# Kernel optimization log

Hardware: AMD Instinct MI355X
Metric: run time of the kernel (lower is better)

## Reference

```python
import jax, jax.numpy as jnp
from jax import lax
import numpy as np

P = 7            # patch_size
NP = 10          # n_patches
WIN = 20         # window_size
STRIDE = 4       # window loop stride
EMB = 128        # embedding_dimension
L = WIN - P + 1  # valid-conv output side (14)
HALF = WIN // 2 - P // 2  # window start offset before clipping (7)


def _positions(H, W):
    # x outer, y inner, exactly matching the nested python loops in the source
    return np.array([(x, y) for x in range(0, H - WIN + 1, STRIDE)
                     for y in range(0, W - WIN + 1, STRIDE)], dtype=np.int32)


def _forward(images, Wp, bp, pos_emb, Wb, bb):
    B, C, H, W = images.shape
    BC = B * C
    pos = jnp.asarray(_positions(H, W))  # [Ppos, 2]

    def per_pos(p):
        x, y = p[0], p[1]
        xb0 = jnp.maximum(x - HALF, 0)          # clipped window start (x / cols)
        yb0 = jnp.maximum(y - HALF, 0)          # clipped window start (y / rows)
        winW = jnp.minimum(x - HALF + WIN, W) - xb0  # clipped window width
        winH = jnp.minimum(y - HALF + WIN, H) - yb0  # clipped window height
        # reference patch: rows y:y+P, cols x:x+P (from ORIGINAL data, as in source)
        ref = lax.dynamic_slice(images, (0, 0, y, x), (B, C, P, P)).reshape(BC, 1, P, P)
        # fixed-size window slice; upper bound never clips for our dims, lower-clip
        # handled by masking invalid candidate offsets below
        win = lax.dynamic_slice(images, (0, 0, yb0, xb0), (B, C, WIN, WIN)).reshape(BC, WIN, WIN)
        # grouped cross-correlation == torch conv2d(groups=BC) similarity
        sim = lax.conv_general_dilated(win[None], ref, (1, 1), 'VALID',
                                       feature_group_count=BC,
                                       dimension_numbers=('NCHW', 'OIHW', 'NCHW'))[0]  # [BC,L,L]
        valid = (jnp.arange(L)[:, None] <= winH - P) & (jnp.arange(L)[None, :] <= winW - P)
        sim = jnp.where(valid[None], sim, -jnp.inf)
        _, idx = lax.top_k(sim.reshape(BC, L * L), NP)  # [BC, NP]
        oy, ox = idx // L, idx % L  # row / col offsets inside the window

        def extract(w2, a, b):
            # source's meshgrid indexing yields the TRANSPOSED patch, flattened
            return lax.dynamic_slice(w2, (a, b), (P, P)).T.reshape(P * P)
        patches = jax.vmap(jax.vmap(extract, in_axes=(None, 0, 0)))(win, oy, ox)  # [BC,NP,P*P]
        # source bug kept: x_coords = row offset + x window start (and vice versa)
        return patches, oy + xb0, ox + yb0

    patches, xi, yi = jax.vmap(per_pos)(pos)  # [Ppos,BC,NP,49], [Ppos,BC,NP] int32 x2

    # NOTE: the TransformerEncoder output is discarded in the source; the actual
    # math is back_projection(projection(patches) + pos_emb).
    emb = patches.reshape(-1, B, C, NP, P * P) @ Wp + bp + pos_emb  # [Ppos,B,C,NP,EMB]
    den = (emb @ Wb + bb).reshape(-1, BC, NP, P, P)                 # [Ppos,BC,NP,P,P]

    img0 = images.reshape(BC, H, W)
    cnt0 = jnp.ones((BC, H, W), images.dtype)

    def upd(im, cn, x_i, y_i, d):
        reg = lax.dynamic_slice(im, (y_i, x_i), (P, P))
        c = lax.dynamic_slice(cn, (y_i, x_i), (P, P))
        im = lax.dynamic_update_slice(im, (reg * c + d) / (c + 1.0), (y_i, x_i))
        # source bug kept: counter incremented at transposed slice [x, y]
        ct = lax.dynamic_slice(cn, (x_i, y_i), (P, P)) + 1.0
        cn = lax.dynamic_update_slice(cn, ct, (x_i, y_i))
        return im, cn
    vupd = jax.vmap(upd)  # (b,c) planes are independent -> vectorize

    def n_step(carry, t):
        d, x_i, y_i = t
        return vupd(carry[0], carry[1], x_i, y_i, d), None

    def pos_step(carry, t):
        d, x_i, y_i = t  # d:[BC,NP,P,P]
        carry, _ = lax.scan(n_step, carry, (jnp.moveaxis(d, 1, 0), x_i.T, y_i.T))
        return carry, None

    (img, _), _ = lax.scan(pos_step, (img0, cnt0), (den, xi, yi))
    return img.reshape(B, C, H, W)


def setup_inputs() -> dict:
    key = jax.random.key(0)
    k0, k1, k2, k3 = jax.random.split(key, 4)
    B, C, H, W = 4, 8, 160, 160
    return {
        'images': jax.random.normal(k0, (B, C, H, W), jnp.float32),
        'Wp': jax.random.normal(k1, (P * P, EMB), jnp.float32) * 0.05,
        'bp': jnp.zeros((EMB,), jnp.float32),
        'pos_emb': jax.random.normal(k2, (1, NP, EMB), jnp.float32),
        'Wb': jax.random.normal(k3, (EMB, P * P), jnp.float32) * 0.05,
        'bb': jnp.zeros((P * P,), jnp.float32),
    }


def reference(images, Wp, bp, pos_emb, Wb, bb):
    return _forward(images, Wp, bp, pos_emb, Wb, bb)
```

## Files before the change

### kernel.cpp

```cpp
#include <hip/hip_runtime.h>

#define PS 7
#define NP 10
#define WIN 20
#define STR 4
#define LL 14
#define HALF 7
#define HH 160
#define WW 160
#define BCN 32
#define NX 36
#define PPOS 1296
#define EMBD 128
#define NTASK (BCN * PPOS * NP)
#define NEV (PPOS * NP)
#define CAP 512
#define NTILE 400

__global__ __launch_bounds__(256) void k_mk(const float* __restrict__ Wp,
                                            const float* __restrict__ bp,
                                            const float* __restrict__ pe,
                                            const float* __restrict__ Wb,
                                            const float* __restrict__ bb,
                                            float* __restrict__ M,
                                            float* __restrict__ K,
                                            unsigned long long* __restrict__ MT) {
    int t = blockIdx.x * 256 + threadIdx.x;
    if (t < 49 * 49) {
        int k = t / 49, d = t % 49;
        float acc = 0.f;
        for (int e = 0; e < EMBD; ++e) acc += Wp[k * EMBD + e] * Wb[e * 49 + d];
        M[t] = acc;
    } else if (t < 49 * 49 + NP * 49) {
        int u = t - 49 * 49;
        int n = u / 49, d = u % 49;
        float acc = bb[d];
        for (int e = 0; e < EMBD; ++e) acc += (bp[e] + pe[n * EMBD + e]) * Wb[e * 49 + d];
        K[u] = acc;
    } else if (t < 49 * 49 + NP * 49 + 256) {
        int u = t - (49 * 49 + NP * 49);
        int ey = (u >> 4) - 7, ex = (u & 15) - 7;
        int r0 = ey > 0 ? ey : 0, r1 = ey + 6 < 7 ? ey + 6 : 7;
        int c0 = ex > 0 ? ex : 0, c1 = ex + 6 < 7 ? ex + 6 : 7;
        unsigned long long m = 0ull;
        if (r0 <= r1 && c0 <= c1) {
            unsigned colp = ((1u << (c1 - c0 + 1)) - 1u) << c0;
            for (int rr = r0; rr <= r1; ++rr)
                m |= (unsigned long long)colp << (8 * rr);
        }
        MT[u] = m;
    }
}

__device__ __forceinline__ float dpp_wave_max(float x) {
    int xi = __float_as_int(x);
#define DPP_STEP(ctrl)                                                          \
    {                                                                           \
        int t_ = __builtin_amdgcn_update_dpp(xi, xi, ctrl, 0xf, 0xf, false);    \
        xi = __float_as_int(fmaxf(__int_as_float(xi), __int_as_float(t_)));     \
    }
    DPP_STEP(0x111)
    DPP_STEP(0x112)
    DPP_STEP(0x114)
    DPP_STEP(0x118)
    DPP_STEP(0x142)
    DPP_STEP(0x143)
#undef DPP_STEP
    return __int_as_float(xi);
}

__global__ __launch_bounds__(256) void k_sim(const float* __restrict__ img,
                                             const float* __restrict__ Mg,
                                             const float* __restrict__ Kg,
                                             unsigned* __restrict__ xy,
                                             float* __restrict__ pd) {
    int tid  = threadIdx.x;
    int wv   = __builtin_amdgcn_readfirstlane(tid >> 6);
    int lane = tid & 63;
    int gt   = blockIdx.x * 4 + wv;
    int pos  = gt % PPOS;
    int bc   = gt / PPOS;
    int ix = pos / NX, iy = pos % NX;
    int x = ix * STR, y = iy * STR;
    int xb0 = max(x - HALF, 0), yb0 = max(y - HALF, 0);
    int jmax = x + 6 - xb0;
    int imax = y + 6 - yb0;
    const float* plane = img + bc * (HH * WW);

    float rf[49];
#pragma unroll
    for (int a = 0; a < PS; ++a)
#pragma unroll
        for (int b = 0; b < PS; ++b)
            rf[a * 7 + b] = plane[(y + a) * WW + (x + b)];

    int B = lane;
    bool bval = B < 56;
    int gr = B / 14, c = B % 14;
    int r0 = gr * 4;
    float acc[4] = {0.f, 0.f, 0.f, 0.f};
    const float* wb = plane + yb0 * WW + xb0 + c;
#pragma unroll
    for (int a = 0; a < 10; ++a) {
        int ra = min(r0 + a, 19);
        const float* rp = wb + ra * WW;
#pragma unroll
        for (int b = 0; b < 7; ++b) {
            float tap = rp[b];
#pragma unroll
            for (int k = 0; k < 4; ++k) {
                int ai = a - k;
                if (ai >= 0 && ai < 7) acc[k] += tap * rf[ai * 7 + b];
            }
        }
    }
    float v[4]; int vidx[4];
#pragma unroll
    for (int k = 0; k < 4; ++k) {
        int rr = r0 + k;
        bool ok = bval && (rr <= imax) && (c <= jmax);
        v[k] = ok ? acc[k] : -INFINITY;
        vidx[k] = rr * 14 + c;
    }

    int ld = min(lane, 48);
    float Mc[49];
#pragma unroll
    for (int j = 0; j < 49; ++j) Mc[j] = Mg[j * 49 + ld];

    bool act = lane < 49;
    int tbase = (bc * PPOS + pos) * NP;

    auto find_and_mask = [&](int& bi_out) {
        float bv = fmaxf(fmaxf(v[0], v[1]), fmaxf(v[2], v[3]));
        bv = dpp_wave_max(bv);
        float bvs = __int_as_float(__builtin_amdgcn_readlane(__float_as_int(bv), 63));
        unsigned long long ms[4];
        ms[0] = __ballot(v[0] == bvs);
        ms[1] = __ballot(v[1] == bvs);
        ms[2] = __ballot(v[2] == bvs);
        ms[3] = __ballot(v[3] == bvs);
        int best = 1 << 30, slotw = 0, lanew = 0;
#pragma unroll
        for (int s = 0; s < 4; ++s) {
            if (ms[s]) {
                int l  = __ffsll(ms[s]) - 1;
                int id = __builtin_amdgcn_readlane(vidx[s], l);
                if (id < best) { best = id; slotw = s; lanew = l; }
            }
        }
#pragma unroll
        for (int s = 0; s < 4; ++s)
            if (s == slotw && lane == lanew) v[s] = -INFINITY;
        bi_out = best;
    };

    int bi;
    find_and_mask(bi);
    for (int n = 0; n < NP; ++n) {
        int oy = bi / 14, ox = bi % 14;
        int x_i = oy + xb0;
        int y_i = ox + yb0;
        int t = tbase + n;
        if (lane == 0) xy[t] = (unsigned)x_i | ((unsigned)y_i << 8);
        const float* src = plane + (yb0 + oy) * WW + (xb0 + ox);

        float tap[49];
#pragma unroll
        for (int j = 0; j < 49; ++j)
            tap[j] = src[(j % 7) * WW + (j / 7)];

        int bi_next = 0;
        if (n < NP - 1) find_and_mask(bi_next);

        float d0 = Kg[n * 49 + ld], d1 = 0.f, d2 = 0.f, d3 = 0.f;
#pragma unroll
        for (int j = 0; j < 48; j += 4) {
            d0 = fmaf(tap[j + 0], Mc[j + 0], d0);
            d1 = fmaf(tap[j + 1], Mc[j + 1], d1);
            d2 = fmaf(tap[j + 2], Mc[j + 2], d2);
            d3 = fmaf(tap[j + 3], Mc[j + 3], d3);
        }
        d0 = fmaf(tap[48], Mc[48], d0);
        float den = (d0 + d1) + (d2 + d3);
        if (act) pd[(size_t)t * 49 + lane] = den;
        bi = bi_next;
    }
}

__global__ __launch_bounds__(256) void k_apply(const float* __restrict__ img,
                                               const unsigned* __restrict__ xy,
                                               const float* __restrict__ pd,
                                               const unsigned long long* __restrict__ mt,
                                               float* __restrict__ out) {
    __shared__ uint2 lsts[4][CAP];
    int tid  = threadIdx.x;
    int wv   = tid >> 6;
    int lane = tid & 63;
    int gt   = blockIdx.x * 4 + wv;
    int bc   = gt / NTILE;
    int tile = gt % NTILE;
    int tx0 = (tile % 20) * 8, ty0 = (tile / 20) * 8;
    int tx1 = tx0 + 7, ty1 = ty0 + 7;
    const unsigned* xs = xy + bc * NEV;
    uint2* lst = lsts[wv];

    int a0 = (tx0 <= 19) ? 0 : ((tx0 - 9) >> 2), a1 = min(35, (tx0 + 14) >> 2);
    int b0 = (ty0 <= 19) ? 0 : ((ty0 - 9) >> 2), b1 = min(35, (ty0 + 14) >> 2);
    if (a0 > b0) { int t0 = a0; a0 = b0; b0 = t0; int t1 = a1; a1 = b1; b1 = t1; }
    int lo0 = a0, lo1 = 0, len0, len1;
    if (b0 <= a1 + 1) { len0 = max(a1, b1) - lo0 + 1; len1 = 0; }
    else              { len0 = a1 - a0 + 1; lo1 = b0; len1 = b1 - b0 + 1; }
    int nU = len0 + len1;
    unsigned m = 65536u / (unsigned)nU + 1u;
    int npos = nU * nU;

    unsigned cnt = 0;
    for (int base = 0; base < npos; base += 64) {
        int k = base + lane;
        bool valid = k < npos;
        unsigned kk = valid ? (unsigned)k : 0u;
        int ki = (int)((kk * m) >> 16);
        int kj = (int)kk - ki * nU;
        int ixp = (ki < len0) ? (lo0 + ki) : (lo1 + ki - len0);
        int iyp = (kj < len0) ? (lo0 + kj) : (lo1 + kj - len0);
        int pos = ixp * NX + iyp;
        const unsigned* ep = xs + pos * NP;

        unsigned ev[NP];
#pragma unroll
        for (int n = 0; n < NP; ++n) ev[n] = ep[n];

        unsigned rel = 0;
        unsigned w0[NP], w1[NP];
#pragma unroll
        for (int n = 0; n < NP; ++n) {
            unsigned u = ev[n];
            int x_i = (int)(u & 255u);
            int y_i = (int)((u >> 8) & 255u);
            bool ih = (x_i <= tx1) && (x_i + 6 >= tx0) &&
                      (y_i <= ty1) && (y_i + 6 >= ty0);
            bool ch = (x_i <= ty1) && (x_i + 6 >= ty0) &&
                      (y_i <= tx1) && (y_i + 6 >= tx0);
            bool any = valid && (ih || ch);
            rel |= any ? (1u << n) : 0u;
            int eyH = y_i - ty0, exH = x_i - tx0;
            int eyC = x_i - ty0, exC = y_i - tx0;
            unsigned hidx = ih ? (unsigned)(((eyH + 7) << 4) | (exH + 7)) : 0u;
            unsigned cidx = ch ? (unsigned)(((eyC + 7) << 4) | (exC + 7)) : 0u;
            unsigned s8q  = ih ? (unsigned)(((7 * eyH + exH) + 48) << 2) : 0u;
            w0[n] = (unsigned)(pos * NP + n);
            w1[n] = hidx | (cidx << 8) | (s8q << 16);
        }
        int myc = __popc(rel);
        int scan = myc;
#pragma unroll
        for (int off = 1; off < 64; off <<= 1) {
            int o = __shfl_up(scan, off);
            scan += (lane >= off) ? o : 0;
        }
        int excl  = (int)cnt + scan - myc;
        int total = __shfl(scan, 63);
        int w = excl;
#pragma unroll
        for (int n = 0; n < NP; ++n) {
            if ((rel >> n) & 1u) { if (w < CAP) lst[w] = make_uint2(w0[n], w1[n]); ++w; }
        }
        cnt += (unsigned)total;
    }
    if (cnt > CAP) cnt = CAP;
    unsigned cntp = (cnt + 7u) & ~7u;
    if (cntp > CAP) cntp = CAP;
    if (lane < (int)(cntp - cnt)) lst[cnt + lane] = make_uint2(0u, 0u);
    int cntN = (int)cntp;

    int r8 = lane >> 3, c8 = lane & 7;
    int r  = ty0 + r8;
    int cc = tx0 + c8;
    float im = img[bc * (HH * WW) + r * WW + cc];
    float c  = 1.0f;
    const float* ds = pd + (size_t)bc * ((size_t)NEV * 49);
    int vOff2 = (r8 * 7 + c8) * 4 + 192;

    for (int i = 0; i < cntN; i += 8) {
        unsigned u0[8], u1[8];
        float    dv[8];
#pragma unroll
        for (int j = 0; j < 8; ++j) {
            uint2 e = lst[i + j];
            u0[j] = (unsigned)__builtin_amdgcn_readfirstlane((int)e.x);
            u1[j] = (unsigned)__builtin_amdgcn_readfirstlane((int)e.y);
        }
#pragma unroll
        for (int j = 0; j < 8; ++j) {
            int t = (int)u0[j];
            const char* dsb = (const char*)(ds + (size_t)t * 49);
            int boc = min(max(vOff2 - (int)((u1[j] >> 16) & 511u), 0), 192);
            dv[j] = *(const float*)(dsb + boc);
        }
        unsigned long long hmv[8], cmv[8];
#pragma unroll
        for (int j = 0; j < 8; ++j) {
            hmv[j] = mt[u1[j] & 255u];
            cmv[j] = mt[(u1[j] >> 8) & 255u];
        }
#pragma unroll
        for (int j = 0; j < 8; ++j) {
            float nim = fmaf(im, c, dv[j]) * __builtin_amdgcn_rcpf(c + 1.0f);
            asm("v_cndmask_b32 %0, %0, %1, %2" : "+v"(im) : "v"(nim), "s"(hmv[j]));
            float inc;
            asm("v_cndmask_b32 %0, 0, 1.0, %1" : "=v"(inc) : "s"(cmv[j]));
            c += inc;
        }
    }
    out[bc * (HH * WW) + r * WW + cc] = im;
}

extern "C" void kernel_launch(void* const* d_in, const int* in_sizes, int n_in,
                              void* d_out, int out_size, void* d_ws, size_t ws_size,
                              hipStream_t stream) {
    const float* img = (const float*)d_in[0];
    const float* Wp  = (const float*)d_in[1];
    const float* bp  = (const float*)d_in[2];
    const float* pe  = (const float*)d_in[3];
    const float* Wb  = (const float*)d_in[4];
    const float* bb  = (const float*)d_in[5];
    float* out = (float*)d_out;

    float* wsf = (float*)d_ws;
    float*              M  = wsf;
    float*              K  = wsf + 2404;
    unsigned long long* MT = (unsigned long long*)(wsf + 2896);
    unsigned*           xy = (unsigned*)(wsf + 3408);
    float*              pd = wsf + 3408 + NTASK;

    k_mk<<<13, 256, 0, stream>>>(Wp, bp, pe, Wb, bb, M, K, MT);
    k_sim<<<BCN * PPOS / 4, 256, 0, stream>>>(img, M, K, xy, pd);
    k_apply<<<BCN * NTILE / 4, 256, 0, stream>>>(img, xy, pd, MT, out);
}
```

Measured before the change: 286.2 us.

## Split denoising matvec out of similarity kernel into per-task thread kernel

The per-patch 49x49 matrix-vector denoise moves out of the similarity/top-k kernel into a new kernel, k_den, where each thread handles one (plane, position, patch) task. There it reads its patch taps and computes all 49 outputs using uniform (broadcast) loads of a transposed M matrix. Results are staged in shared memory so the global stores are coalesced. This lightens the wave-per-position sim kernel and removes its serial per-patch work. The cost is an extra launch, re-reading the patch from global memory, and 49 sequential output loops per thread with high register use.

```diff
diff --git a/kernel.cpp b/kernel.cpp
--- a/kernel.cpp
+++ b/kernel.cpp
@@ -22,15 +22,15 @@
                                             const float* __restrict__ pe,
                                             const float* __restrict__ Wb,
                                             const float* __restrict__ bb,
-                                            float* __restrict__ M,
+                                            float* __restrict__ M2,
                                             float* __restrict__ K,
                                             unsigned long long* __restrict__ MT) {
     int t = blockIdx.x * 256 + threadIdx.x;
     if (t < 49 * 49) {
-        int k = t / 49, d = t % 49;
+        int d = t / 49, j = t % 49;
         float acc = 0.f;
-        for (int e = 0; e < EMBD; ++e) acc += Wp[k * EMBD + e] * Wb[e * 49 + d];
-        M[t] = acc;
+        for (int e = 0; e < EMBD; ++e) acc += Wp[j * EMBD + e] * Wb[e * 49 + d];
+        M2[t] = acc;
     } else if (t < 49 * 49 + NP * 49) {
         int u = t - 49 * 49;
         int n = u / 49, d = u % 49;
@@ -70,10 +70,7 @@
 }
 
 __global__ __launch_bounds__(256) void k_sim(const float* __restrict__ img,
-                                             const float* __restrict__ Mg,
-                                             const float* __restrict__ Kg,
-                                             unsigned* __restrict__ xy,
-                                             float* __restrict__ pd) {
+                                             unsigned* __restrict__ xy) {
     int tid  = threadIdx.x;
     int wv   = __builtin_amdgcn_readfirstlane(tid >> 6);
     int lane = tid & 63;
@@ -123,15 +120,9 @@
         vidx[k] = rr * 14 + c;
     }
 
-    int ld = min(lane, 48);
-    float Mc[49];
-#pragma unroll
-    for (int j = 0; j < 49; ++j) Mc[j] = Mg[j * 49 + ld];
-
-    bool act = lane < 49;
     int tbase = (bc * PPOS + pos) * NP;
 
-    auto find_and_mask = [&](int& bi_out) {
+    for (int n = 0; n < NP; ++n) {
         float bv = fmaxf(fmaxf(v[0], v[1]), fmaxf(v[2], v[3]));
         bv = dpp_wave_max(bv);
         float bvs = __int_as_float(__builtin_amdgcn_readlane(__float_as_int(bv), 63));
@@ -152,40 +143,56 @@
 #pragma unroll
         for (int s = 0; s < 4; ++s)
             if (s == slotw && lane == lanew) v[s] = -INFINITY;
-        bi_out = best;
-    };
-
-    int bi;
-    find_and_mask(bi);
-    for (int n = 0; n < NP; ++n) {
-        int oy = bi / 14, ox = bi % 14;
+
+        int oy = best / 14, ox = best % 14;
         int x_i = oy + xb0;
         int y_i = ox + yb0;
-        int t = tbase + n;
-        if (lane == 0) xy[t] = (unsigned)x_i | ((unsigned)y_i << 8);
-        const float* src = plane + (yb0 + oy) * WW + (xb0 + ox);
-
-        float tap[49];
-#pragma unroll
-        for (int j = 0; j < 49; ++j)
-            tap[j] = src[(j % 7) * WW + (j / 7)];
-
-        int bi_next = 0;
-        if (n < NP - 1) find_and_mask(bi_next);
-
-        float d0 = Kg[n * 49 + ld], d1 = 0.f, d2 = 0.f, d3 = 0.f;
-#pragma unroll
-        for (int j = 0; j < 48; j += 4) {
-            d0 = fmaf(tap[j + 0], Mc[j + 0], d0);
-            d1 = fmaf(tap[j + 1], Mc[j + 1], d1);
-            d2 = fmaf(tap[j + 2], Mc[j + 2], d2);
-            d3 = fmaf(tap[j + 3], Mc[j + 3], d3);
-        }
-        d0 = fmaf(tap[48], Mc[48], d0);
-        float den = (d0 + d1) + (d2 + d3);
-        if (act) pd[(size_t)t * 49 + lane] = den;
-        bi = bi_next;
-    }
+        if (lane == 0) xy[tbase + n] = (unsigned)x_i | ((unsigned)y_i << 8);
+    }
+}
+
+__global__ __launch_bounds__(256) void k_den(const float* __restrict__ img,
+                                             const unsigned* __restrict__ xy,
+                                             const float* __restrict__ M2,
+                                             const float* __restrict__ Kg,
+                                             float* __restrict__ pd) {
+    __shared__ float xb[4][64 * 49];
+    int tid  = threadIdx.x;
+    int wv   = tid >> 6;
+    int lane = tid & 63;
+    int t = blockIdx.x * 256 + tid;
+    int n = t % NP;
+    int q = t / NP;
+    int pos = q % PPOS;
+    int bc  = q / PPOS;
+    int ix = pos / NX, iy = pos % NX;
+    int x = ix * STR, y = iy * STR;
+    int xb0 = max(x - HALF, 0), yb0 = max(y - HALF, 0);
+    unsigned u = xy[t];
+    int x_i = (int)(u & 255u), y_i = (int)((u >> 8) & 255u);
+    const float* src = img + bc * (HH * WW) + (yb0 + x_i - xb0) * WW + (xb0 + y_i - yb0);
+
+    float tap[49];
+#pragma unroll
+    for (int j = 0; j < 49; ++j) tap[j] = src[(j % 7) * WW + (j / 7)];
+
+    const float* kp = Kg + n * 49;
+    float* xbuf = xb[wv];
+    for (int d = 0; d < 49; ++d) {
+        const float* mrow = M2 + d * 49;
+        float a0 = 0.f, a1 = 0.f;
+#pragma unroll
+        for (int j = 0; j < 48; j += 2) {
+            a0 = fmaf(tap[j],     mrow[j],     a0);
+            a1 = fmaf(tap[j + 1], mrow[j + 1], a1);
+        }
+        a0 = fmaf(tap[48], mrow[48], a0);
+        xbuf[lane * 49 + d] = (a0 + a1) + kp[d];
+    }
+    size_t base = (size_t)(blockIdx.x * 256 + wv * 64) * 49;
+#pragma unroll
+    for (int i = 0; i < 49; ++i)
+        pd[base + i * 64 + lane] = xbuf[i * 64 + lane];
 }
 
 __global__ __launch_bounds__(256) void k_apply(const float* __restrict__ img,
@@ -328,13 +335,14 @@
     float* out = (float*)d_out;
 
     float* wsf = (float*)d_ws;
-    float*              M  = wsf;
+    float*              M2 = wsf;
     float*              K  = wsf + 2404;
     unsigned long long* MT = (unsigned long long*)(wsf + 2896);
     unsigned*           xy = (unsigned*)(wsf + 3408);
     float*              pd = wsf + 3408 + NTASK;
 
-    k_mk<<<13, 256, 0, stream>>>(Wp, bp, pe, Wb, bb, M, K, MT);
-    k_sim<<<BCN * PPOS / 4, 256, 0, stream>>>(img, M, K, xy, pd);
+    k_mk<<<13, 256, 0, stream>>>(Wp, bp, pe, Wb, bb, M2, K, MT);
+    k_sim<<<BCN * PPOS / 4, 256, 0, stream>>>(img, xy);
+    k_den<<<NTASK / 256, 256, 0, stream>>>(img, xy, M2, K, pd);
     k_apply<<<BCN * NTILE / 4, 256, 0, stream>>>(img, xy, pd, MT, out);
 }
```

Measured after the change: 287.6 us. No clear change (+0.5%).
